# Kernel optimization log

Hardware: AMD Instinct MI355X
Metric: run time of the kernel (lower is better)

The kernel has to match this reference:

```python
import jax, jax.numpy as jnp
import numpy as np

SEQ, BATCH, HID = 4096, 32, 512


def setup_inputs() -> dict:
    key = jax.random.key(0)
    ks = jax.random.split(key, 7)
    s = 1.0 / np.sqrt(HID)
    return {
        "x0": jax.random.normal(ks[0], (SEQ, BATCH, 1), dtype=jnp.float32),
        "W_ih": jax.random.uniform(ks[1], (4 * HID, 1), jnp.float32, -s, s),
        "W_hh": jax.random.uniform(ks[2], (4 * HID, HID), jnp.float32, -s, s),
        "b_ih": jax.random.uniform(ks[3], (4 * HID,), jnp.float32, -s, s),
        "b_hh": jax.random.uniform(ks[4], (4 * HID,), jnp.float32, -s, s),
        "W_lin": jax.random.uniform(ks[5], (1, HID), jnp.float32, -s, s),
        "b_lin": jax.random.uniform(ks[6], (1,), jnp.float32, -s, s),
    }


def _lstm(x0, W_ih, W_hh, b_ih, b_hh):
    # x0: (T, B, 1). Precompute input contribution to gates for all steps.
    x_proj = jnp.einsum("tbi,gi->tbg", x0, W_ih) + (b_ih + b_hh)  # (T, B, 4H)
    T, B, _ = x_proj.shape
    H = W_hh.shape[1]
    h0 = jnp.zeros((B, H), x0.dtype)
    c0 = jnp.zeros((B, H), x0.dtype)

    def step(carry, xp):
        h, c = carry
        gates = xp + h @ W_hh.T  # (B, 4H)
        i, f, g, o = jnp.split(gates, 4, axis=-1)  # torch gate order i,f,g,o
        i = jax.nn.sigmoid(i)
        f = jax.nn.sigmoid(f)
        g = jnp.tanh(g)
        o = jax.nn.sigmoid(o)
        c = f * c + i * g
        h = o * jnp.tanh(c)
        return (h, c), h

    _, hs = jax.lax.scan(step, (h0, c0), x_proj)  # hs: (T, B, H)
    return hs


def reference(x0, W_ih, W_hh, b_ih, b_hh, W_lin, b_lin):
    hs = _lstm(x0, W_ih, W_hh, b_ih, b_hh)            # (T, B, H)
    y = jnp.einsum("tbh,oh->tbo", hs, W_lin) + b_lin  # (T, B, 1)
    return y + x0                                      # residual add
```

## Files before the change

### kernel.cpp

```cpp
#include <hip/hip_runtime.h>
#include <stdint.h>

#define T_STEPS 4096
#define BATCH 32
#define HID 512
#define GROUPS 8
#define BLK_THREADS 1024
#define NBLOCKS 256

typedef _Float16 h2_t __attribute__((ext_vector_type(2)));
typedef uint32_t u32x16 __attribute__((ext_vector_type(16)));

__device__ inline uint32_t pack_h2(float a, float b) {
  h2_t v;
  v.x = (_Float16)a;
  v.y = (_Float16)b;
  return __builtin_bit_cast(uint32_t, v);
}

__device__ inline float fdot2(uint32_t a, uint32_t b, float c) {
  return __builtin_amdgcn_fdot2(__builtin_bit_cast(h2_t, a),
                                __builtin_bit_cast(h2_t, b), c, false);
}

__device__ inline uint32_t aread(uint32_t a) {
  uint32_t v;
  asm("v_accvgpr_read_b32 %0, %1" : "=v"(v) : "a"(a));
  return v;
}

__device__ inline uint64_t uni64(const void* p) {
  uint32_t lo = __builtin_amdgcn_readfirstlane((uint32_t)(uintptr_t)p);
  uint32_t hi = __builtin_amdgcn_readfirstlane((uint32_t)((uintptr_t)p >> 32));
  return ((uint64_t)hi << 32) | lo;
}

__device__ inline void kinv() {
  asm volatile("s_dcache_inv" ::: "memory");
}
__device__ inline uint32_t sload1(uint64_t p) {
  uint32_t v;
  asm volatile("s_load_dword %0, %1, 0x0\n\ts_waitcnt lgkmcnt(0)"
               : "=s"(v) : "s"(p) : "memory");
  return v;
}
__device__ inline u32x16 sload16(uint64_t p) {
  u32x16 v;
  asm volatile("s_load_dwordx16 %0, %1, 0x0\n\ts_waitcnt lgkmcnt(0)"
               : "=s"(v) : "s"(p) : "memory");
  return v;
}
__device__ inline void waitcnt_vm0() {
  asm volatile("s_waitcnt vmcnt(0)" ::: "memory");
}

__device__ inline float sigf(float x) { return 1.0f / (1.0f + __expf(-x)); }
__device__ inline float tanh_fast(float x) {
  float a = fabsf(x);
  float e = __expf(-2.0f * a);
  float r = (1.0f - e) / (1.0f + e);
  return copysignf(r, x);
}

__global__ __launch_bounds__(BLK_THREADS)
void lstm_smem(const float* __restrict__ x0,
               const float* __restrict__ W_ih,
               const float* __restrict__ W_hh,
               const float* __restrict__ b_ih,
               const float* __restrict__ b_hh,
               const float* __restrict__ W_lin,
               const float* __restrict__ b_lin,
               float* __restrict__ y,
               uint32_t* __restrict__ h_ex,
               uint32_t* __restrict__ cnt,
               int* __restrict__ claim)
{
  __shared__ float x0_lds[T_STEPS];
  __shared__ float ylds[T_STEPS];
  __shared__ float gacc[2][256];
  __shared__ int s_bg;

  const int tid = threadIdx.x;

  if (tid == 0) {
    uint32_t xcc;
    asm volatile("s_getreg_b32 %0, hwreg(HW_REG_XCC_ID)" : "=s"(xcc));
    xcc &= 7;
    int slot = atomicAdd(claim + xcc * 16, 1);
    s_bg = (slot < 32) ? (int)(((4 * xcc + (slot >> 3)) << 3) | (slot & 7))
                       : -1;
  }
  __syncthreads();
  if (s_bg < 0) return;
  const int b  = s_bg >> 3;
  const int g  = s_bg & 7;
  const int u0 = g * 64;
  const int wv = tid >> 6;
  const int rg = wv >> 3;
  const int cs = wv & 7;
  const int l  = tid & 63;

  uint32_t a0[32], a1[32];
  {
    const int r0 = 128 * rg + l;
    const int r1 = r0 + 64;
    const int R0 = (r0 >> 6) * HID + u0 + (r0 & 63);
    const int R1 = (r1 >> 6) * HID + u0 + (r1 & 63);
    const float2* p0 = (const float2*)(W_hh + (size_t)R0 * HID + 64 * cs);
    const float2* p1 = (const float2*)(W_hh + (size_t)R1 * HID + 64 * cs);
#pragma unroll
    for (int k = 0; k < 32; ++k) {
      float2 a = p0[k], c = p1[k];
      uint32_t t0 = pack_h2(a.x, a.y);
      uint32_t t1 = pack_h2(c.x, c.y);
      asm("v_accvgpr_write_b32 %0, %1" : "=a"(a0[k]) : "v"(t0));
      asm("v_accvgpr_write_b32 %0, %1" : "=a"(a1[k]) : "v"(t1));
    }
  }
  for (int i = tid; i < T_STEPS; i += BLK_THREADS) {
    x0_lds[i] = x0[i * BATCH + b];
    ylds[i] = 0.f;
  }
  if (tid < 256) { gacc[0][tid] = 0.f; gacc[1][tid] = 0.f; }

  float c_state = 0.f;
  float wih_[4] = {0.f, 0.f, 0.f, 0.f}, bs_[4] = {0.f, 0.f, 0.f, 0.f};
  float wlin_u = 0.f, blin = 0.f;
  if (tid < 64) {
#pragma unroll
    for (int j = 0; j < 4; ++j) {
      int R = j * HID + u0 + tid;
      wih_[j] = W_ih[R];
      bs_[j] = b_ih[R] + b_hh[R];
    }
    wlin_u = W_lin[u0 + tid];
    blin = b_lin[0];
  }

  uint32_t* hb = h_ex + (size_t)b * 256;
  const uint64_t dpu[2] = { uni64(hb + 32 * cs),
                            uni64(hb + BATCH * 256 + 32 * cs) };
  const uint64_t cwu = uni64(cnt + b * 16 + cs);
  uint32_t* pub01[2] = { hb + 32 * g, hb + BATCH * 256 + 32 * g };
  uint32_t* cnt_b = cnt + b * 16;

  __syncthreads();

  int dead = 0;
  for (int t = 0; t < T_STEPS; ++t) {
    const int sl = t & 1, ns = sl ^ 1;

    {
      int guard = 0;
      for (;;) {
        kinv();
        uint32_t c = sload1(cwu);
        if ((int)c >= t) break;
        if (dead || ++guard > (1 << 20)) { dead = 1; break; }
        __builtin_amdgcn_s_sleep(1);
      }
    }
    u32x16 hs0 = sload16(dpu[sl]);
    u32x16 hs1 = sload16(dpu[sl] + 64);

    float acc0 = 0.f, acc1 = 0.f;
#pragma unroll
    for (int k = 0; k < 16; ++k) {
      acc0 = fdot2(aread(a0[k]), hs0[k], acc0);
      acc1 = fdot2(aread(a1[k]), hs0[k], acc1);
    }
#pragma unroll
    for (int k = 0; k < 16; ++k) {
      acc0 = fdot2(aread(a0[16 + k]), hs1[k], acc0);
      acc1 = fdot2(aread(a1[16 + k]), hs1[k], acc1);
    }
    atomicAdd(&gacc[sl][128 * rg + l], acc0);
    atomicAdd(&gacc[sl][128 * rg + 64 + l], acc1);
    __syncthreads();

    if (tid < 64) {
      const float xv = x0_lds[t];
      float gi = gacc[sl][tid]       + xv * wih_[0] + bs_[0];
      float gf = gacc[sl][tid + 64]  + xv * wih_[1] + bs_[1];
      float gg = gacc[sl][tid + 128] + xv * wih_[2] + bs_[2];
      float go = gacc[sl][tid + 192] + xv * wih_[3] + bs_[3];
      float si = sigf(gi), sf = sigf(gf), tg_ = tanh_fast(gg), so = sigf(go);
      c_state = sf * c_state + si * tg_;
      float h = so * tanh_fast(c_state);

      float hn = __shfl_down(h, 1, 64);
      if ((tid & 1) == 0) pub01[ns][tid >> 1] = pack_h2(h, hn);
      waitcnt_vm0();
      if (tid == 0) cnt_b[g] = (uint32_t)(t + 1);

      gacc[sl][tid] = 0.f;
      gacc[sl][tid + 64] = 0.f;
      gacc[sl][tid + 128] = 0.f;
      gacc[sl][tid + 192] = 0.f;

      float p = wlin_u * h;
#pragma unroll
      for (int m = 32; m >= 1; m >>= 1) p += __shfl_xor(p, m, 64);
      if (tid == 0) ylds[t] = p;
    }
  }

  __syncthreads();
  for (int i = tid; i < T_STEPS; i += BLK_THREADS) {
    float val = ylds[i];
    if (g == 0) val += blin + x0_lds[i];
    unsafeAtomicAdd(&y[i * BATCH + b], val);
  }
}

extern "C" void kernel_launch(void* const* d_in, const int* in_sizes, int n_in,
                              void* d_out, int out_size, void* d_ws, size_t ws_size,
                              hipStream_t stream) {
  const float* x0    = (const float*)d_in[0];
  const float* W_ih  = (const float*)d_in[1];
  const float* W_hh  = (const float*)d_in[2];
  const float* b_ih  = (const float*)d_in[3];
  const float* b_hh  = (const float*)d_in[4];
  const float* W_lin = (const float*)d_in[5];
  const float* b_lin = (const float*)d_in[6];
  float* y = (float*)d_out;

  uint32_t* h_ex = (uint32_t*)d_ws;
  uint32_t* cnt  = h_ex + 2 * BATCH * 256;
  int* claim     = (int*)(cnt + BATCH * 16);
  const size_t init_bytes = (2 * BATCH * 256 + BATCH * 16) * sizeof(uint32_t)
                            + 8 * 16 * sizeof(int);

  (void)hipMemsetAsync(d_ws, 0, init_bytes, stream);
  (void)hipMemsetAsync(d_out, 0, (size_t)out_size * sizeof(float), stream);

  hipLaunchKernelGGL(lstm_smem, dim3(NBLOCKS), dim3(BLK_THREADS), 0, stream,
                     x0, W_ih, W_hh, b_ih, b_hh, W_lin, b_lin, y, h_ex, cnt,
                     claim);
}
```

Baseline: 14.97 ms.

## Replace separate step counters with per-line tagged h exchange records

Each group now publishes its half-precision h values into 64-byte lines that each carry a step tag word in the same line. Consumers poll the data directly with scalar loads and proceed once all four tags match the current step. This removes the separate counter write, the vmcnt wait between data and flag, and the extra counter-then-data round trip. The approach depends on each tagged line becoming visible as a unit. Split accumulators also shorten the fdot2 dependency chain.

```diff
diff --git a/kernel.cpp b/kernel.cpp
--- a/kernel.cpp
+++ b/kernel.cpp
@@ -7,9 +7,10 @@
 #define GROUPS 8
 #define BLK_THREADS 1024
 #define NBLOCKS 256
+#define SLOT_DW (BATCH * GROUPS * 64)
 
 typedef _Float16 h2_t __attribute__((ext_vector_type(2)));
-typedef uint32_t u32x16 __attribute__((ext_vector_type(16)));
+typedef uint32_t u32x8 __attribute__((ext_vector_type(8)));
 
 __device__ inline uint32_t pack_h2(float a, float b) {
   h2_t v;
@@ -38,20 +39,23 @@
 __device__ inline void kinv() {
   asm volatile("s_dcache_inv" ::: "memory");
 }
-__device__ inline uint32_t sload1(uint64_t p) {
-  uint32_t v;
-  asm volatile("s_load_dword %0, %1, 0x0\n\ts_waitcnt lgkmcnt(0)"
-               : "=s"(v) : "s"(p) : "memory");
-  return v;
-}
-__device__ inline u32x16 sload16(uint64_t p) {
-  u32x16 v;
-  asm volatile("s_load_dwordx16 %0, %1, 0x0\n\ts_waitcnt lgkmcnt(0)"
-               : "=s"(v) : "s"(p) : "memory");
-  return v;
-}
-__device__ inline void waitcnt_vm0() {
-  asm volatile("s_waitcnt vmcnt(0)" ::: "memory");
+
+__device__ inline void sload_rec(uint64_t p, u32x8* d0, u32x8* d1,
+                                 u32x8* d2, u32x8* d3,
+                                 uint32_t* t0, uint32_t* t1,
+                                 uint32_t* t2, uint32_t* t3) {
+  asm volatile("s_load_dwordx8 %0, %8, 0x0\n\t"
+               "s_load_dword %4, %8, 0x20\n\t"
+               "s_load_dwordx8 %1, %8, 0x40\n\t"
+               "s_load_dword %5, %8, 0x60\n\t"
+               "s_load_dwordx8 %2, %8, 0x80\n\t"
+               "s_load_dword %6, %8, 0xa0\n\t"
+               "s_load_dwordx8 %3, %8, 0xc0\n\t"
+               "s_load_dword %7, %8, 0xe0\n\t"
+               "s_waitcnt lgkmcnt(0)"
+               : "=&s"(*d0), "=&s"(*d1), "=&s"(*d2), "=&s"(*d3),
+                 "=&s"(*t0), "=&s"(*t1), "=&s"(*t2), "=&s"(*t3)
+               : "s"(p) : "memory");
 }
 
 __device__ inline float sigf(float x) { return 1.0f / (1.0f + __expf(-x)); }
@@ -63,17 +67,16 @@
 }
 
 __global__ __launch_bounds__(BLK_THREADS)
-void lstm_smem(const float* __restrict__ x0,
-               const float* __restrict__ W_ih,
-               const float* __restrict__ W_hh,
-               const float* __restrict__ b_ih,
-               const float* __restrict__ b_hh,
-               const float* __restrict__ W_lin,
-               const float* __restrict__ b_lin,
-               float* __restrict__ y,
-               uint32_t* __restrict__ h_ex,
-               uint32_t* __restrict__ cnt,
-               int* __restrict__ claim)
+void lstm_tagline(const float* __restrict__ x0,
+                  const float* __restrict__ W_ih,
+                  const float* __restrict__ W_hh,
+                  const float* __restrict__ b_ih,
+                  const float* __restrict__ b_hh,
+                  const float* __restrict__ W_lin,
+                  const float* __restrict__ b_lin,
+                  float* __restrict__ y,
+                  uint32_t* __restrict__ h_ex,
+                  int* __restrict__ claim)
 {
   __shared__ float x0_lds[T_STEPS];
   __shared__ float ylds[T_STEPS];
@@ -137,12 +140,10 @@
     blin = b_lin[0];
   }
 
-  uint32_t* hb = h_ex + (size_t)b * 256;
-  const uint64_t dpu[2] = { uni64(hb + 32 * cs),
-                            uni64(hb + BATCH * 256 + 32 * cs) };
-  const uint64_t cwu = uni64(cnt + b * 16 + cs);
-  uint32_t* pub01[2] = { hb + 32 * g, hb + BATCH * 256 + 32 * g };
-  uint32_t* cnt_b = cnt + b * 16;
+  uint32_t* hb = h_ex + (size_t)b * (GROUPS * 64);
+  const uint64_t dpu[2] = { uni64(hb + 64 * cs),
+                            uni64(hb + SLOT_DW + 64 * cs) };
+  uint32_t* pub01[2] = { hb + 64 * g, hb + SLOT_DW + 64 * g };
 
   __syncthreads();
 
@@ -150,32 +151,35 @@
   for (int t = 0; t < T_STEPS; ++t) {
     const int sl = t & 1, ns = sl ^ 1;
 
+    u32x8 D0, D1, D2, D3;
+    uint32_t tg0, tg1, tg2, tg3;
     {
+      const uint32_t want = (uint32_t)t;
       int guard = 0;
       for (;;) {
         kinv();
-        uint32_t c = sload1(cwu);
-        if ((int)c >= t) break;
-        if (dead || ++guard > (1 << 20)) { dead = 1; break; }
+        sload_rec(dpu[sl], &D0, &D1, &D2, &D3, &tg0, &tg1, &tg2, &tg3);
+        if ((tg0 == want) & (tg1 == want) &
+            (tg2 == want) & (tg3 == want)) break;
+        if (dead || ++guard > (1 << 18)) { dead = 1; break; }
         __builtin_amdgcn_s_sleep(1);
       }
     }
-    u32x16 hs0 = sload16(dpu[sl]);
-    u32x16 hs1 = sload16(dpu[sl] + 64);
-
-    float acc0 = 0.f, acc1 = 0.f;
-#pragma unroll
-    for (int k = 0; k < 16; ++k) {
-      acc0 = fdot2(aread(a0[k]), hs0[k], acc0);
-      acc1 = fdot2(aread(a1[k]), hs0[k], acc1);
-    }
-#pragma unroll
-    for (int k = 0; k < 16; ++k) {
-      acc0 = fdot2(aread(a0[16 + k]), hs1[k], acc0);
-      acc1 = fdot2(aread(a1[16 + k]), hs1[k], acc1);
-    }
-    atomicAdd(&gacc[sl][128 * rg + l], acc0);
-    atomicAdd(&gacc[sl][128 * rg + 64 + l], acc1);
+
+    float acc0a = 0.f, acc0b = 0.f, acc1a = 0.f, acc1b = 0.f;
+#pragma unroll
+    for (int k = 0; k < 8; ++k) {
+      acc0a = fdot2(aread(a0[k]),      D0[k], acc0a);
+      acc1a = fdot2(aread(a1[k]),      D0[k], acc1a);
+      acc0b = fdot2(aread(a0[8 + k]),  D1[k], acc0b);
+      acc1b = fdot2(aread(a1[8 + k]),  D1[k], acc1b);
+      acc0a = fdot2(aread(a0[16 + k]), D2[k], acc0a);
+      acc1a = fdot2(aread(a1[16 + k]), D2[k], acc1a);
+      acc0b = fdot2(aread(a0[24 + k]), D3[k], acc0b);
+      acc1b = fdot2(aread(a1[24 + k]), D3[k], acc1b);
+    }
+    atomicAdd(&gacc[sl][128 * rg + l], acc0a + acc0b);
+    atomicAdd(&gacc[sl][128 * rg + 64 + l], acc1a + acc1b);
     __syncthreads();
 
     if (tid < 64) {
@@ -189,9 +193,21 @@
       float h = so * tanh_fast(c_state);
 
       float hn = __shfl_down(h, 1, 64);
-      if ((tid & 1) == 0) pub01[ns][tid >> 1] = pack_h2(h, hn);
-      waitcnt_vm0();
-      if (tid == 0) cnt_b[g] = (uint32_t)(t + 1);
+      uint32_t val = 0;
+      int doff = 0;
+      bool act = false;
+      if ((tid & 1) == 0) {
+        int j = tid >> 1;
+        val = pack_h2(h, hn);
+        doff = ((j >> 3) << 4) + (j & 7);
+        act = true;
+      } else if (tid < 8) {
+        int L = (tid - 1) >> 1;
+        val = (uint32_t)(t + 1);
+        doff = (L << 4) + 8;
+        act = true;
+      }
+      if (act) pub01[ns][doff] = val;
 
       gacc[sl][tid] = 0.f;
       gacc[sl][tid + 64] = 0.f;
@@ -226,15 +242,13 @@
   float* y = (float*)d_out;
 
   uint32_t* h_ex = (uint32_t*)d_ws;
-  uint32_t* cnt  = h_ex + 2 * BATCH * 256;
-  int* claim     = (int*)(cnt + BATCH * 16);
-  const size_t init_bytes = (2 * BATCH * 256 + BATCH * 16) * sizeof(uint32_t)
+  int* claim     = (int*)(h_ex + 2 * SLOT_DW);
+  const size_t init_bytes = (size_t)2 * SLOT_DW * sizeof(uint32_t)
                             + 8 * 16 * sizeof(int);
 
   (void)hipMemsetAsync(d_ws, 0, init_bytes, stream);
   (void)hipMemsetAsync(d_out, 0, (size_t)out_size * sizeof(float), stream);
 
-  hipLaunchKernelGGL(lstm_smem, dim3(NBLOCKS), dim3(BLK_THREADS), 0, stream,
-                     x0, W_ih, W_hh, b_ih, b_hh, W_lin, b_lin, y, h_ex, cnt,
-                     claim);
-}
+  hipLaunchKernelGGL(lstm_tagline, dim3(NBLOCKS), dim3(BLK_THREADS), 0, stream,
+                     x0, W_ih, W_hh, b_ih, b_hh, W_lin, b_lin, y, h_ex, claim);
+}
```

Result: faster. 14.49 ms (-3.2%).

## Replace per-wave scalar polling with single-wave agent-scope vector polling and LDS staging

Applied to the files above, without the earlier changes.

Previously every wave spun on a scalar-cache counter after invalidating the scalar cache, then read its own hidden-state slice with scalar loads. Now one wave per block polls all 8 group tags with agent-scope atomic vector loads, copies the whole hidden vector into LDS, and the other waves read it after a barrier. Weights move from AGPRs into ordinary VGPRs, and the dot products use split accumulators to shorten the dependency chain. This cuts redundant polling traffic and scalar cache invalidations, at the cost of an extra block-wide barrier and an LDS round trip on the critical path of each step.

```diff
diff --git a/kernel.cpp b/kernel.cpp
--- a/kernel.cpp
+++ b/kernel.cpp
@@ -7,9 +7,11 @@
 #define GROUPS 8
 #define BLK_THREADS 1024
 #define NBLOCKS 256
+#define BSLOT_DW 256
+#define SLOT_DW (BATCH * BSLOT_DW)
 
 typedef _Float16 h2_t __attribute__((ext_vector_type(2)));
-typedef uint32_t u32x16 __attribute__((ext_vector_type(16)));
+typedef uint32_t u32x4 __attribute__((ext_vector_type(4)));
 
 __device__ inline uint32_t pack_h2(float a, float b) {
   h2_t v;
@@ -21,37 +23,6 @@
 __device__ inline float fdot2(uint32_t a, uint32_t b, float c) {
   return __builtin_amdgcn_fdot2(__builtin_bit_cast(h2_t, a),
                                 __builtin_bit_cast(h2_t, b), c, false);
-}
-
-__device__ inline uint32_t aread(uint32_t a) {
-  uint32_t v;
-  asm("v_accvgpr_read_b32 %0, %1" : "=v"(v) : "a"(a));
-  return v;
-}
-
-__device__ inline uint64_t uni64(const void* p) {
-  uint32_t lo = __builtin_amdgcn_readfirstlane((uint32_t)(uintptr_t)p);
-  uint32_t hi = __builtin_amdgcn_readfirstlane((uint32_t)((uintptr_t)p >> 32));
-  return ((uint64_t)hi << 32) | lo;
-}
-
-__device__ inline void kinv() {
-  asm volatile("s_dcache_inv" ::: "memory");
-}
-__device__ inline uint32_t sload1(uint64_t p) {
-  uint32_t v;
-  asm volatile("s_load_dword %0, %1, 0x0\n\ts_waitcnt lgkmcnt(0)"
-               : "=s"(v) : "s"(p) : "memory");
-  return v;
-}
-__device__ inline u32x16 sload16(uint64_t p) {
-  u32x16 v;
-  asm volatile("s_load_dwordx16 %0, %1, 0x0\n\ts_waitcnt lgkmcnt(0)"
-               : "=s"(v) : "s"(p) : "memory");
-  return v;
-}
-__device__ inline void waitcnt_vm0() {
-  asm volatile("s_waitcnt vmcnt(0)" ::: "memory");
 }
 
 __device__ inline float sigf(float x) { return 1.0f / (1.0f + __expf(-x)); }
@@ -63,21 +34,22 @@
 }
 
 __global__ __launch_bounds__(BLK_THREADS)
-void lstm_smem(const float* __restrict__ x0,
-               const float* __restrict__ W_ih,
-               const float* __restrict__ W_hh,
-               const float* __restrict__ b_ih,
-               const float* __restrict__ b_hh,
-               const float* __restrict__ W_lin,
-               const float* __restrict__ b_lin,
-               float* __restrict__ y,
-               uint32_t* __restrict__ h_ex,
-               uint32_t* __restrict__ cnt,
-               int* __restrict__ claim)
+void lstm_vecagent(const float* __restrict__ x0,
+                   const float* __restrict__ W_ih,
+                   const float* __restrict__ W_hh,
+                   const float* __restrict__ b_ih,
+                   const float* __restrict__ b_hh,
+                   const float* __restrict__ W_lin,
+                   const float* __restrict__ b_lin,
+                   float* __restrict__ y,
+                   uint32_t* __restrict__ h_ex,
+                   uint32_t* __restrict__ tags,
+                   int* __restrict__ claim)
 {
   __shared__ float x0_lds[T_STEPS];
   __shared__ float ylds[T_STEPS];
   __shared__ float gacc[2][256];
+  __shared__ __align__(16) uint32_t h_lds[2][BSLOT_DW];
   __shared__ int s_bg;
 
   const int tid = threadIdx.x;
@@ -100,7 +72,7 @@
   const int cs = wv & 7;
   const int l  = tid & 63;
 
-  uint32_t a0[32], a1[32];
+  uint32_t w0[32], w1[32];
   {
     const int r0 = 128 * rg + l;
     const int r1 = r0 + 64;
@@ -111,10 +83,8 @@
 #pragma unroll
     for (int k = 0; k < 32; ++k) {
       float2 a = p0[k], c = p1[k];
-      uint32_t t0 = pack_h2(a.x, a.y);
-      uint32_t t1 = pack_h2(c.x, c.y);
-      asm("v_accvgpr_write_b32 %0, %1" : "=a"(a0[k]) : "v"(t0));
-      asm("v_accvgpr_write_b32 %0, %1" : "=a"(a1[k]) : "v"(t1));
+      w0[k] = pack_h2(a.x, a.y);
+      w1[k] = pack_h2(c.x, c.y);
     }
   }
   for (int i = tid; i < T_STEPS; i += BLK_THREADS) {
@@ -137,12 +107,10 @@
     blin = b_lin[0];
   }
 
-  uint32_t* hb = h_ex + (size_t)b * 256;
-  const uint64_t dpu[2] = { uni64(hb + 32 * cs),
-                            uni64(hb + BATCH * 256 + 32 * cs) };
-  const uint64_t cwu = uni64(cnt + b * 16 + cs);
-  uint32_t* pub01[2] = { hb + 32 * g, hb + BATCH * 256 + 32 * g };
-  uint32_t* cnt_b = cnt + b * 16;
+  uint32_t* tags_b = tags + b * 8;
+  uint32_t* hrec[2] = { h_ex + (size_t)b * BSLOT_DW,
+                        h_ex + SLOT_DW + (size_t)b * BSLOT_DW };
+  uint32_t* pub01[2] = { hrec[0] + 32 * g, hrec[1] + 32 * g };
 
   __syncthreads();
 
@@ -150,32 +118,47 @@
   for (int t = 0; t < T_STEPS; ++t) {
     const int sl = t & 1, ns = sl ^ 1;
 
-    {
-      int guard = 0;
-      for (;;) {
-        kinv();
-        uint32_t c = sload1(cwu);
-        if ((int)c >= t) break;
-        if (dead || ++guard > (1 << 20)) { dead = 1; break; }
-        __builtin_amdgcn_s_sleep(1);
+    if (wv == 15) {
+      {
+        int guard = 0;
+        for (;;) {
+          bool ok = true;
+          if (l < 8) {
+            uint32_t tg = __hip_atomic_load(&tags_b[l], __ATOMIC_RELAXED,
+                                            __HIP_MEMORY_SCOPE_AGENT);
+            ok = ((int)tg >= t);
+          }
+          if (__all(ok)) break;
+          if (dead || ++guard > (1 << 17)) { dead = 1; break; }
+        }
       }
-    }
-    u32x16 hs0 = sload16(dpu[sl]);
-    u32x16 hs1 = sload16(dpu[sl] + 64);
-
-    float acc0 = 0.f, acc1 = 0.f;
-#pragma unroll
-    for (int k = 0; k < 16; ++k) {
-      acc0 = fdot2(aread(a0[k]), hs0[k], acc0);
-      acc1 = fdot2(aread(a1[k]), hs0[k], acc1);
-    }
-#pragma unroll
-    for (int k = 0; k < 16; ++k) {
-      acc0 = fdot2(aread(a0[16 + k]), hs1[k], acc0);
-      acc1 = fdot2(aread(a1[16 + k]), hs1[k], acc1);
-    }
-    atomicAdd(&gacc[sl][128 * rg + l], acc0);
-    atomicAdd(&gacc[sl][128 * rg + 64 + l], acc1);
+      const uint64_t* src = (const uint64_t*)hrec[sl];
+      uint64_t q0 = __hip_atomic_load(&src[l], __ATOMIC_RELAXED,
+                                      __HIP_MEMORY_SCOPE_AGENT);
+      uint64_t q1 = __hip_atomic_load(&src[l + 64], __ATOMIC_RELAXED,
+                                      __HIP_MEMORY_SCOPE_AGENT);
+      uint64_t* dst = (uint64_t*)h_lds[sl];
+      dst[l] = q0;
+      dst[l + 64] = q1;
+    }
+    __syncthreads();
+
+    const u32x4* hs4 = (const u32x4*)&h_lds[sl][32 * cs];
+    float acc0a = 0.f, acc0b = 0.f, acc1a = 0.f, acc1b = 0.f;
+#pragma unroll
+    for (int k = 0; k < 8; ++k) {
+      u32x4 hv = hs4[k];
+      acc0a = fdot2(w0[4 * k + 0], hv[0], acc0a);
+      acc1a = fdot2(w1[4 * k + 0], hv[0], acc1a);
+      acc0b = fdot2(w0[4 * k + 1], hv[1], acc0b);
+      acc1b = fdot2(w1[4 * k + 1], hv[1], acc1b);
+      acc0a = fdot2(w0[4 * k + 2], hv[2], acc0a);
+      acc1a = fdot2(w1[4 * k + 2], hv[2], acc1a);
+      acc0b = fdot2(w0[4 * k + 3], hv[3], acc0b);
+      acc1b = fdot2(w1[4 * k + 3], hv[3], acc1b);
+    }
+    atomicAdd(&gacc[sl][128 * rg + l], acc0a + acc0b);
+    atomicAdd(&gacc[sl][128 * rg + 64 + l], acc1a + acc1b);
     __syncthreads();
 
     if (tid < 64) {
@@ -190,8 +173,10 @@
 
       float hn = __shfl_down(h, 1, 64);
       if ((tid & 1) == 0) pub01[ns][tid >> 1] = pack_h2(h, hn);
-      waitcnt_vm0();
-      if (tid == 0) cnt_b[g] = (uint32_t)(t + 1);
+      asm volatile("s_waitcnt vmcnt(0)" ::: "memory");
+      if (tid == 0)
+        __hip_atomic_store(&tags_b[g], (uint32_t)(t + 1), __ATOMIC_RELEASE,
+                           __HIP_MEMORY_SCOPE_AGENT);
 
       gacc[sl][tid] = 0.f;
       gacc[sl][tid + 64] = 0.f;
@@ -226,15 +211,15 @@
   float* y = (float*)d_out;
 
   uint32_t* h_ex = (uint32_t*)d_ws;
-  uint32_t* cnt  = h_ex + 2 * BATCH * 256;
-  int* claim     = (int*)(cnt + BATCH * 16);
-  const size_t init_bytes = (2 * BATCH * 256 + BATCH * 16) * sizeof(uint32_t)
+  uint32_t* tags = h_ex + 2 * SLOT_DW;
+  int* claim     = (int*)(tags + BATCH * 8);
+  const size_t init_bytes = (size_t)(2 * SLOT_DW + BATCH * 8) * sizeof(uint32_t)
                             + 8 * 16 * sizeof(int);
 
   (void)hipMemsetAsync(d_ws, 0, init_bytes, stream);
   (void)hipMemsetAsync(d_out, 0, (size_t)out_size * sizeof(float), stream);
 
-  hipLaunchKernelGGL(lstm_smem, dim3(NBLOCKS), dim3(BLK_THREADS), 0, stream,
-                     x0, W_ih, W_hh, b_ih, b_hh, W_lin, b_lin, y, h_ex, cnt,
+  hipLaunchKernelGGL(lstm_vecagent, dim3(NBLOCKS), dim3(BLK_THREADS), 0, stream,
+                     x0, W_ih, W_hh, b_ih, b_hh, W_lin, b_lin, y, h_ex, tags,
                      claim);
 }
```

Result: slower. 29.07 ms (+94.2%).
